# Optimization experiments

Measured on AMD Instinct MI355X. Metric: run time of the kernel, lower is better.

The kernel has to match this reference:

```python
import jax, jax.numpy as jnp
import numpy as np

N_HEADS = 16
D_MODEL = 1024
D_K = D_MODEL // N_HEADS


def setup_inputs() -> dict:
    key = jax.random.key(0)
    ks = jax.random.split(key, 9)
    B, L = 4, 2048
    s = 1.0 / np.sqrt(D_MODEL)
    x = jax.random.normal(ks[0], (B, L, D_MODEL), dtype=jnp.float32)
    mask = jnp.tril(jnp.ones((L, L), dtype=jnp.int32))  # causal [L, L]
    Wq = jax.random.normal(ks[1], (D_MODEL, D_MODEL), dtype=jnp.float32) * s
    Wk = jax.random.normal(ks[2], (D_MODEL, D_MODEL), dtype=jnp.float32) * s
    Wv = jax.random.normal(ks[3], (D_MODEL, D_MODEL), dtype=jnp.float32) * s
    Wo = jax.random.normal(ks[4], (D_MODEL, D_MODEL), dtype=jnp.float32) * s
    bq = jnp.zeros((D_MODEL,), jnp.float32)
    bk = jnp.zeros((D_MODEL,), jnp.float32)
    bv = jnp.zeros((D_MODEL,), jnp.float32)
    bo = jnp.zeros((D_MODEL,), jnp.float32)
    return {"x": x, "mask": mask, "Wq": Wq, "bq": bq, "Wk": Wk, "bk": bk,
            "Wv": Wv, "bv": bv, "Wo": Wo, "bo": bo}


def reference(x, mask, Wq, bq, Wk, bk, Wv, bv, Wo, bo):
    B, L, _ = x.shape
    # projections -> [B, H, L, d_k]
    def split_heads(t):
        return t.reshape(B, L, N_HEADS, D_K).transpose(0, 2, 1, 3)
    Q = split_heads(x @ Wq + bq)
    K = split_heads(x @ Wk + bk)
    V = split_heads(x @ Wv + bv)
    orig_dtype = Q.dtype
    # fp32 upcast for scores (faithful to source)
    scores = jnp.einsum('bhqd,bhkd->bhqk', Q.astype(jnp.float32),
                        K.astype(jnp.float32)) / np.sqrt(D_K)
    # orig dtype is float32 -> masked fill with -inf
    scores = jnp.where(mask == 0, -jnp.inf, scores).astype(orig_dtype)
    attn = jax.nn.softmax(scores, axis=-1)  # dropout p=0 -> identity (eval)
    out = jnp.einsum('bhqk,bhkd->bhqd', attn, V)
    out = out.transpose(0, 2, 1, 3).reshape(B, L, D_MODEL)
    return out @ Wo + bo
```

## Files before the change

### kernel.cpp

```cpp
#include <hip/hip_runtime.h>

#define DMODEL 1024
#define NTOK   8192
#define SEQ    2048
#define NH     16
#define DK     64

typedef short short8  __attribute__((ext_vector_type(8)));
typedef short short4v __attribute__((ext_vector_type(4)));
typedef float floatx4 __attribute__((ext_vector_type(4)));

__device__ __forceinline__ unsigned short f2bf(float f) {
  unsigned int u = __float_as_uint(f);
  u += 0x7fffu + ((u >> 16) & 1u);
  return (unsigned short)(u >> 16);
}

__device__ __forceinline__ void async16(short* lds, const short* g) {
  __builtin_amdgcn_global_load_lds(
      (const __attribute__((address_space(1))) void*)g,
      (__attribute__((address_space(3))) void*)lds, 16, 0, 0);
}

__global__ void cast_x_kernel(const float4* __restrict__ x, ushort4* __restrict__ o, int n4) {
  int i = blockIdx.x * 256 + threadIdx.x;
  if (i < n4) {
    float4 v = x[i];
    ushort4 u;
    u.x = f2bf(v.x); u.y = f2bf(v.y); u.z = f2bf(v.z); u.w = f2bf(v.w);
    o[i] = u;
  }
}

__global__ void transpose_cast4(const float* __restrict__ W0, const float* __restrict__ W1,
                                const float* __restrict__ W2, const float* __restrict__ W3,
                                short* __restrict__ T0, short* __restrict__ T1,
                                short* __restrict__ T2, short* __restrict__ T3) {
  __shared__ float tile[32][33];
  const int z = blockIdx.z;
  const float* W = (z == 0) ? W0 : (z == 1) ? W1 : (z == 2) ? W2 : W3;
  short*      Wt = (z == 0) ? T0 : (z == 1) ? T1 : (z == 2) ? T2 : T3;
  int bx = blockIdx.x, by = blockIdx.y;
  int tx = threadIdx.x, ty = threadIdx.y;
#pragma unroll
  for (int j = 0; j < 4; ++j)
    tile[ty + j * 8][tx] = W[(size_t)(by * 32 + ty + j * 8) * DMODEL + bx * 32 + tx];
  __syncthreads();
#pragma unroll
  for (int j = 0; j < 4; ++j)
    Wt[(size_t)(bx * 32 + ty + j * 8) * DMODEL + by * 32 + tx] =
        (short)f2bf(tile[tx][ty + j * 8]);
}

__global__ __launch_bounds__(256) void transpose_v(const short* __restrict__ Vb,
                                                   short* __restrict__ Vt) {
  __shared__ short t[64][72];
  const int bh = blockIdx.y, l0 = blockIdx.x * 64;
  const int tid = threadIdx.x;
  const int r = tid >> 2, c0 = (tid & 3) * 16;
  const short* src = Vb + (size_t)bh * SEQ * DK + (size_t)(l0 + r) * DK + c0;
  *(short8*)&t[r][c0]     = *(const short8*)src;
  *(short8*)&t[r][c0 + 8] = *(const short8*)(src + 8);
  __syncthreads();
  short tmp[16];
#pragma unroll
  for (int j = 0; j < 16; ++j) tmp[j] = t[c0 + j][r];
  short* dst = Vt + (size_t)bh * DK * SEQ + (size_t)r * SEQ + l0 + c0;
  *(short8*)dst       = *(const short8*)tmp;
  *(short8*)(dst + 8) = *(const short8*)(tmp + 8);
}

__device__ __forceinline__ void gemm_core(const short* __restrict__ A,
                                          const short* __restrict__ Bt,
                                          int m0, int n0, short* lds,
                                          floatx4 acc[4][4]) {
  const int tid  = threadIdx.x;
  const int lane = tid & 63, w = tid >> 6;
  const int wm = w >> 1, wn = w & 1;
  const int ln = lane & 15, quad = lane >> 4;
  short* As = lds;
  short* Bs = lds + 4096;
  const int   srow = tid >> 2;
  const int   scol = (tid & 3) * 8;
  const short* ga = A  + (size_t)(m0 + srow) * DMODEL + scol;
  const short* gb = Bt + (size_t)(n0 + srow) * DMODEL + scol;
  short* la = As + w * 512;
  short* lb = Bs + w * 512;
  for (int kb = 0; kb < DMODEL; kb += 32) {
    __syncthreads();
    async16(la,        ga + kb);
    async16(la + 2048, ga + (size_t)64 * DMODEL + kb);
    async16(lb,        gb + kb);
    async16(lb + 2048, gb + (size_t)64 * DMODEL + kb);
    __syncthreads();
    short8 af[4], bf[4];
#pragma unroll
    for (int t = 0; t < 4; ++t) {
      af[t] = *(const short8*)(As + (wm * 64 + t * 16 + ln) * 32 + quad * 8);
      bf[t] = *(const short8*)(Bs + (wn * 64 + t * 16 + ln) * 32 + quad * 8);
    }
#pragma unroll
    for (int mt = 0; mt < 4; ++mt)
#pragma unroll
      for (int nt = 0; nt < 4; ++nt)
        acc[mt][nt] = __builtin_amdgcn_mfma_f32_16x16x32_bf16(af[mt], bf[nt], acc[mt][nt], 0, 0, 0);
  }
}

__global__ __launch_bounds__(256) void gemm_qkv(
    const short* __restrict__ xb,
    const short* __restrict__ Wqt, const short* __restrict__ Wkt, const short* __restrict__ Wvt,
    const float* __restrict__ bq,  const float* __restrict__ bk,  const float* __restrict__ bv,
    short* __restrict__ Qb, short* __restrict__ Kb, short* __restrict__ Vb) {
  __shared__ __align__(16) short lds[8192];
  const int z = blockIdx.z;
  const short* Wt   = (z == 0) ? Wqt : (z == 1) ? Wkt : Wvt;
  const float* bias = (z == 0) ? bq  : (z == 1) ? bk  : bv;
  short* out        = (z == 0) ? Qb  : (z == 1) ? Kb  : Vb;
  const float scale = (z == 0) ? 0.18033688011112042f : 1.0f;
  const int m0 = blockIdx.y * 128, n0 = blockIdx.x * 128;
  floatx4 acc[4][4];
#pragma unroll
  for (int i = 0; i < 4; ++i)
#pragma unroll
    for (int j = 0; j < 4; ++j) acc[i][j] = (floatx4){0.f, 0.f, 0.f, 0.f};
  gemm_core(xb, Wt, m0, n0, lds, acc);
  const int tid = threadIdx.x, lane = tid & 63, w = tid >> 6;
  const int wm = w >> 1, wn = w & 1, ln = lane & 15, quad = lane >> 4;
#pragma unroll
  for (int mt = 0; mt < 4; ++mt)
#pragma unroll
    for (int nt = 0; nt < 4; ++nt) {
      int n = n0 + wn * 64 + nt * 16 + ln;
      float bb = bias[n];
      int h = n >> 6, d = n & 63;
#pragma unroll
      for (int r = 0; r < 4; ++r) {
        int m = m0 + wm * 64 + mt * 16 + quad * 4 + r;
        float v = (acc[mt][nt][r] + bb) * scale;
        int b = m >> 11, l = m & 2047;
        out[(size_t)(b * NH + h) * (SEQ * DK) + (size_t)l * DK + d] = (short)f2bf(v);
      }
    }
}

__global__ __launch_bounds__(256) void gemm_out(
    const short* __restrict__ Ob, const short* __restrict__ Wot,
    const float* __restrict__ bo, float* __restrict__ outp) {
  __shared__ __align__(16) short lds[8192];
  const int m0 = blockIdx.y * 128, n0 = blockIdx.x * 128;
  floatx4 acc[4][4];
#pragma unroll
  for (int i = 0; i < 4; ++i)
#pragma unroll
    for (int j = 0; j < 4; ++j) acc[i][j] = (floatx4){0.f, 0.f, 0.f, 0.f};
  gemm_core(Ob, Wot, m0, n0, lds, acc);
  const int tid = threadIdx.x, lane = tid & 63, w = tid >> 6;
  const int wm = w >> 1, wn = w & 1, ln = lane & 15, quad = lane >> 4;
#pragma unroll
  for (int mt = 0; mt < 4; ++mt)
#pragma unroll
    for (int nt = 0; nt < 4; ++nt) {
      int n = n0 + wn * 64 + nt * 16 + ln;
      float bb = bo[n];
#pragma unroll
      for (int r = 0; r < 4; ++r) {
        int m = m0 + wm * 64 + mt * 16 + quad * 4 + r;
        outp[(size_t)m * DMODEL + n] = acc[mt][nt][r] + bb;
      }
    }
}

#define FMAX 12.0f

__device__ __forceinline__ void attn_tile(
    const short* __restrict__ Ksb, const short* __restrict__ Vsb,
    short* __restrict__ Psg, const short8 qf[2][2],
    floatx4 acc[4][2], float lst[2],
    int qbase, int kt, int ln, int quad, int w) {
  floatx4 s[4][2];
#pragma unroll
  for (int i = 0; i < 4; ++i)
#pragma unroll
    for (int j = 0; j < 2; ++j) s[i][j] = (floatx4){0.f, 0.f, 0.f, 0.f};
#pragma unroll
  for (int kk = 0; kk < 2; ++kk) {
    short8 kf[4];
#pragma unroll
    for (int t = 0; t < 4; ++t)
      kf[t] = *(const short8*)(Ksb + (t * 16 + ln) * 64 + ((kk * 4 + quad) ^ (ln & 7)) * 8);
#pragma unroll
    for (int t = 0; t < 4; ++t)
#pragma unroll
      for (int qt = 0; qt < 2; ++qt)
        s[t][qt] = __builtin_amdgcn_mfma_f32_16x16x32_bf16(kf[t], qf[qt][kk], s[t][qt], 0, 0, 0);
  }
  if (kt * 64 + 63 > qbase) {
#pragma unroll
    for (int t = 0; t < 4; ++t)
#pragma unroll
      for (int qt = 0; qt < 2; ++qt)
#pragma unroll
        for (int r = 0; r < 4; ++r) {
          int kg = kt * 64 + t * 16 + quad * 4 + r;
          int qg = qbase + w * 32 + qt * 16 + ln;
          if (kg > qg) s[t][qt][r] = -1.0e30f;
        }
  }
#pragma unroll
  for (int qt = 0; qt < 2; ++qt) {
    float rs = 0.f;
#pragma unroll
    for (int t = 0; t < 4; ++t) {
      short4v pk;
#pragma unroll
      for (int r = 0; r < 4; ++r) {
        float p = __builtin_amdgcn_exp2f(s[t][qt][r] - FMAX);
        rs += p;
        pk[r] = (short)f2bf(p);
      }
      *(short4v*)(Psg + (w * 32 + qt * 16 + ln) * 72 + t * 16 + quad * 4) = pk;
    }
    lst[qt] += rs;
  }
  __threadfence_block();
#pragma unroll
  for (int kk = 0; kk < 2; ++kk) {
    short8 vf[4], pf[2];
#pragma unroll
    for (int dt = 0; dt < 4; ++dt)
      vf[dt] = *(const short8*)(Vsb + (dt * 16 + ln) * 64 + ((kk * 4 + quad) ^ (ln & 7)) * 8);
#pragma unroll
    for (int qt = 0; qt < 2; ++qt)
      pf[qt] = *(const short8*)(Psg + (w * 32 + qt * 16 + ln) * 72 + kk * 32 + quad * 8);
#pragma unroll
    for (int dt = 0; dt < 4; ++dt)
#pragma unroll
      for (int qt = 0; qt < 2; ++qt)
        acc[dt][qt] = __builtin_amdgcn_mfma_f32_16x16x32_bf16(vf[dt], pf[qt], acc[dt][qt], 0, 0, 0);
  }
}

__global__ __launch_bounds__(256, 2) void attn_kernel(
    const short* __restrict__ Qb, const short* __restrict__ Kb,
    const short* __restrict__ Vt, short* __restrict__ Ob) {
  __shared__ __align__(16) short Ks[2][64 * 64];
  __shared__ __align__(16) short Vs[2][64 * 64];
  __shared__ __align__(16) short Ps[2][128 * 72];
  const int tid = threadIdx.x, lane = tid & 63, w = tid >> 6;
  const int ln = lane & 15, quad = lane >> 4;
  const int pr  = blockIdx.x;
  const int qt0L = pr, qt0H = 15 - pr;
  const int bh  = blockIdx.y;
  const short* Qh = Qb + (size_t)bh * (SEQ * DK);
  const short* Kh = Kb + (size_t)bh * (SEQ * DK);
  const short* Vh = Vt + (size_t)bh * (DK * SEQ);

  short8 qfL[2][2], qfH[2][2];
#pragma unroll
  for (int qt = 0; qt < 2; ++qt)
#pragma unroll
    for (int kk = 0; kk < 2; ++kk) {
      qfL[qt][kk] = *(const short8*)(Qh +
          (size_t)(qt0L * 128 + w * 32 + qt * 16 + ln) * DK + kk * 32 + quad * 8);
      qfH[qt][kk] = *(const short8*)(Qh +
          (size_t)(qt0H * 128 + w * 32 + qt * 16 + ln) * DK + kk * 32 + quad * 8);
    }

  floatx4 accL[4][2], accH[4][2];
#pragma unroll
  for (int i = 0; i < 4; ++i)
#pragma unroll
    for (int j = 0; j < 2; ++j) {
      accL[i][j] = (floatx4){0.f, 0.f, 0.f, 0.f};
      accH[i][j] = (floatx4){0.f, 0.f, 0.f, 0.f};
    }
  float lstL[2] = {0.f, 0.f}, lstH[2] = {0.f, 0.f};

  const int lr = lane >> 3, fch = (lane & 7) ^ lr;
  const int nkt = 2 * qt0H + 2;
  const int nlt = 2 * qt0L + 2;

#pragma unroll
  for (int i = 0; i < 2; ++i) {
    int row = w * 16 + i * 8;
    async16(&Ks[0][row * 64], Kh + (size_t)(row + lr) * DK + fch * 8);
    async16(&Vs[0][row * 64], Vh + (size_t)(row + lr) * SEQ + fch * 8);
  }
  for (int kt = 0; kt < nkt; ++kt) {
    const int cur = kt & 1;
    __syncthreads();
    if (kt + 1 < nkt) {
      const short* Kt = Kh + (size_t)(kt + 1) * 64 * DK;
#pragma unroll
      for (int i = 0; i < 2; ++i) {
        int row = w * 16 + i * 8;
        async16(&Ks[cur ^ 1][row * 64], Kt + (size_t)(row + lr) * DK + fch * 8);
        async16(&Vs[cur ^ 1][row * 64],
                Vh + (size_t)(row + lr) * SEQ + (kt + 1) * 64 + fch * 8);
      }
    }
    if (kt < nlt)
      attn_tile(Ks[cur], Vs[cur], Ps[0], qfL, accL, lstL, qt0L * 128, kt, ln, quad, w);
    attn_tile(Ks[cur], Vs[cur], Ps[1], qfH, accH, lstH, qt0H * 128, kt, ln, quad, w);
  }

#pragma unroll
  for (int qt = 0; qt < 2; ++qt) {
    float lL = lstL[qt];
    lL += __shfl_xor(lL, 16); lL += __shfl_xor(lL, 32);
    float lH = lstH[qt];
    lH += __shfl_xor(lH, 16); lH += __shfl_xor(lH, 32);
    float invL = 1.0f / lL, invH = 1.0f / lH;
#pragma unroll
    for (int dt = 0; dt < 4; ++dt) {
      short4v oL, oH;
#pragma unroll
      for (int r = 0; r < 4; ++r) {
        oL[r] = (short)f2bf(accL[dt][qt][r] * invL);
        oH[r] = (short)f2bf(accH[dt][qt][r] * invH);
      }
      *(short4v*)(Ps[0] + (w * 32 + qt * 16 + ln) * 72 + dt * 16 + quad * 4) = oL;
      *(short4v*)(Ps[1] + (w * 32 + qt * 16 + ln) * 72 + dt * 16 + quad * 4) = oH;
    }
  }
  __syncthreads();
  const int b = bh >> 4, h = bh & 15;
  const int row = tid >> 1, c0 = (tid & 1) * 32;
  {
    short* dst = Ob + (size_t)(b * SEQ + qt0L * 128 + row) * DMODEL + h * DK + c0;
    const short* srcp = Ps[0] + row * 72 + c0;
#pragma unroll
    for (int u = 0; u < 4; ++u) *(short8*)(dst + u * 8) = *(const short8*)(srcp + u * 8);
  }
  {
    short* dst = Ob + (size_t)(b * SEQ + qt0H * 128 + row) * DMODEL + h * DK + c0;
    const short* srcp = Ps[1] + row * 72 + c0;
#pragma unroll
    for (int u = 0; u < 4; ++u) *(short8*)(dst + u * 8) = *(const short8*)(srcp + u * 8);
  }
}

extern "C" void kernel_launch(void* const* d_in, const int* in_sizes, int n_in,
                              void* d_out, int out_size, void* d_ws, size_t ws_size,
                              hipStream_t stream) {
  (void)in_sizes; (void)n_in; (void)out_size; (void)ws_size;
  const float* x  = (const float*)d_in[0];
  const float* Wq = (const float*)d_in[2];
  const float* bq = (const float*)d_in[3];
  const float* Wk = (const float*)d_in[4];
  const float* bk = (const float*)d_in[5];
  const float* Wv = (const float*)d_in[6];
  const float* bv = (const float*)d_in[7];
  const float* Wo = (const float*)d_in[8];
  const float* bo = (const float*)d_in[9];

  char* ws = (char*)d_ws;
  short* xb  = (short*)(ws);
  short* Vtg = (short*)(ws);
  short* Wqt = (short*)(ws + ((size_t)16 << 20));
  short* Wkt = (short*)(ws + ((size_t)18 << 20));
  short* Wvt = (short*)(ws + ((size_t)20 << 20));
  short* Wot = (short*)(ws + ((size_t)22 << 20));
  short* Qb  = (short*)(ws + ((size_t)24 << 20));
  short* Kb  = (short*)(ws + ((size_t)40 << 20));
  short* Vb  = (short*)(ws + ((size_t)56 << 20));
  short* Ob  = (short*)(ws + ((size_t)72 << 20));

  cast_x_kernel<<<NTOK * DMODEL / 4 / 256, 256, 0, stream>>>(
      (const float4*)x, (ushort4*)xb, NTOK * DMODEL / 4);
  transpose_cast4<<<dim3(32, 32, 4), dim3(32, 8), 0, stream>>>(
      Wq, Wk, Wv, Wo, Wqt, Wkt, Wvt, Wot);

  gemm_qkv<<<dim3(DMODEL / 128, NTOK / 128, 3), 256, 0, stream>>>(
      xb, Wqt, Wkt, Wvt, bq, bk, bv, Qb, Kb, Vb);

  transpose_v<<<dim3(SEQ / 64, 4 * NH), 256, 0, stream>>>(Vb, Vtg);

  attn_kernel<<<dim3(8, 4 * NH), 256, 0, stream>>>(Qb, Kb, Vtg, Ob);

  gemm_out<<<dim3(DMODEL / 128, NTOK / 128), 256, 0, stream>>>(Ob, Wot, bo, (float*)d_out);
}
```

Baseline: 292.8 us.

## Fuse Q/K/V projections into one GEMM and write V transposed directly

Replaces the three-way z-grid QKV GEMM with a single kernel that loads each x tile once and computes Q, K and V accumulators together, sharing the A fragment across three B tiles. The V epilogue writes straight into the transposed [B,H,DK,L] layout with packed 4-element stores, which removes the separate transpose_v kernel and its extra round trip through memory. The fused kernel holds 192 accumulator floats per thread and uses more LDS, so register pressure and occupancy are a risk. The grid also shrinks from 1536 to 512 blocks.

```diff
diff --git a/kernel.cpp b/kernel.cpp
--- a/kernel.cpp
+++ b/kernel.cpp
@@ -52,38 +52,118 @@
         (short)f2bf(tile[tx][ty + j * 8]);
 }
 
-__global__ __launch_bounds__(256) void transpose_v(const short* __restrict__ Vb,
-                                                   short* __restrict__ Vt) {
-  __shared__ short t[64][72];
-  const int bh = blockIdx.y, l0 = blockIdx.x * 64;
-  const int tid = threadIdx.x;
-  const int r = tid >> 2, c0 = (tid & 3) * 16;
-  const short* src = Vb + (size_t)bh * SEQ * DK + (size_t)(l0 + r) * DK + c0;
-  *(short8*)&t[r][c0]     = *(const short8*)src;
-  *(short8*)&t[r][c0 + 8] = *(const short8*)(src + 8);
-  __syncthreads();
-  short tmp[16];
-#pragma unroll
-  for (int j = 0; j < 16; ++j) tmp[j] = t[c0 + j][r];
-  short* dst = Vt + (size_t)bh * DK * SEQ + (size_t)r * SEQ + l0 + c0;
-  *(short8*)dst       = *(const short8*)tmp;
-  *(short8*)(dst + 8) = *(const short8*)(tmp + 8);
-}
-
-__device__ __forceinline__ void gemm_core(const short* __restrict__ A,
-                                          const short* __restrict__ Bt,
-                                          int m0, int n0, short* lds,
-                                          floatx4 acc[4][4]) {
-  const int tid  = threadIdx.x;
-  const int lane = tid & 63, w = tid >> 6;
-  const int wm = w >> 1, wn = w & 1;
-  const int ln = lane & 15, quad = lane >> 4;
+__global__ __launch_bounds__(256, 2) void gemm_qkv_fused(
+    const short* __restrict__ xb,
+    const short* __restrict__ Wqt, const short* __restrict__ Wkt, const short* __restrict__ Wvt,
+    const float* __restrict__ bq,  const float* __restrict__ bk,  const float* __restrict__ bv,
+    short* __restrict__ Qb, short* __restrict__ Kb, short* __restrict__ Vt) {
+  __shared__ __align__(16) short As[4096];
+  __shared__ __align__(16) short Bs[3][4096];
+  const int tid = threadIdx.x, lane = tid & 63, w = tid >> 6;
+  const int wm = w >> 1, wn = w & 1, ln = lane & 15, quad = lane >> 4;
+  const int m0 = blockIdx.y * 128, n0 = blockIdx.x * 128;
+
+  floatx4 acc[3][4][4];
+#pragma unroll
+  for (int z = 0; z < 3; ++z)
+#pragma unroll
+    for (int i = 0; i < 4; ++i)
+#pragma unroll
+      for (int j = 0; j < 4; ++j) acc[z][i][j] = (floatx4){0.f, 0.f, 0.f, 0.f};
+
+  const int srow = tid >> 2, scol = (tid & 3) * 8;
+  const short* ga  = xb  + (size_t)(m0 + srow) * DMODEL + scol;
+  const short* gb0 = Wqt + (size_t)(n0 + srow) * DMODEL + scol;
+  const short* gb1 = Wkt + (size_t)(n0 + srow) * DMODEL + scol;
+  const short* gb2 = Wvt + (size_t)(n0 + srow) * DMODEL + scol;
+  short* la  = As    + w * 512;
+  short* lb0 = Bs[0] + w * 512;
+  short* lb1 = Bs[1] + w * 512;
+  short* lb2 = Bs[2] + w * 512;
+
+  for (int kb = 0; kb < DMODEL; kb += 32) {
+    __syncthreads();
+    async16(la,         ga  + kb);
+    async16(la  + 2048, ga  + (size_t)64 * DMODEL + kb);
+    async16(lb0,        gb0 + kb);
+    async16(lb0 + 2048, gb0 + (size_t)64 * DMODEL + kb);
+    async16(lb1,        gb1 + kb);
+    async16(lb1 + 2048, gb1 + (size_t)64 * DMODEL + kb);
+    async16(lb2,        gb2 + kb);
+    async16(lb2 + 2048, gb2 + (size_t)64 * DMODEL + kb);
+    __syncthreads();
+    short8 af[4];
+#pragma unroll
+    for (int t = 0; t < 4; ++t)
+      af[t] = *(const short8*)(As + (wm * 64 + t * 16 + ln) * 32 + quad * 8);
+#pragma unroll
+    for (int z = 0; z < 3; ++z) {
+      short8 bf[4];
+#pragma unroll
+      for (int t = 0; t < 4; ++t)
+        bf[t] = *(const short8*)(Bs[z] + (wn * 64 + t * 16 + ln) * 32 + quad * 8);
+#pragma unroll
+      for (int mt = 0; mt < 4; ++mt)
+#pragma unroll
+        for (int nt = 0; nt < 4; ++nt)
+          acc[z][mt][nt] = __builtin_amdgcn_mfma_f32_16x16x32_bf16(af[mt], bf[nt], acc[z][mt][nt], 0, 0, 0);
+    }
+  }
+
+#pragma unroll
+  for (int z = 0; z < 2; ++z) {
+    const float* bias = z ? bk : bq;
+    short* out        = z ? Kb : Qb;
+    const float scale = z ? 1.0f : 0.18033688011112042f;
+#pragma unroll
+    for (int mt = 0; mt < 4; ++mt)
+#pragma unroll
+      for (int nt = 0; nt < 4; ++nt) {
+        int n = n0 + wn * 64 + nt * 16 + ln;
+        float bb = bias[n];
+        int h = n >> 6, d = n & 63;
+#pragma unroll
+        for (int r = 0; r < 4; ++r) {
+          int m = m0 + wm * 64 + mt * 16 + quad * 4 + r;
+          int b = m >> 11, l = m & 2047;
+          out[(size_t)(b * NH + h) * (SEQ * DK) + (size_t)l * DK + d] =
+              (short)f2bf((acc[z][mt][nt][r] + bb) * scale);
+        }
+      }
+  }
+#pragma unroll
+  for (int mt = 0; mt < 4; ++mt)
+#pragma unroll
+    for (int nt = 0; nt < 4; ++nt) {
+      int n = n0 + wn * 64 + nt * 16 + ln;
+      float bb = bv[n];
+      int h = n >> 6, d = n & 63;
+      int mb = m0 + wm * 64 + mt * 16 + quad * 4;
+      int b = mb >> 11, l = mb & 2047;
+      short4v pk;
+#pragma unroll
+      for (int r = 0; r < 4; ++r) pk[r] = (short)f2bf(acc[2][mt][nt][r] + bb);
+      *(short4v*)(Vt + ((size_t)(b * NH + h) * DK + d) * SEQ + l) = pk;
+    }
+}
+
+__global__ __launch_bounds__(256) void gemm_out(
+    const short* __restrict__ Ob, const short* __restrict__ Wot,
+    const float* __restrict__ bo, float* __restrict__ outp) {
+  __shared__ __align__(16) short lds[8192];
+  const int tid = threadIdx.x, lane = tid & 63, w = tid >> 6;
+  const int wm = w >> 1, wn = w & 1, ln = lane & 15, quad = lane >> 4;
+  const int m0 = blockIdx.y * 128, n0 = blockIdx.x * 128;
+  floatx4 acc[4][4];
+#pragma unroll
+  for (int i = 0; i < 4; ++i)
+#pragma unroll
+    for (int j = 0; j < 4; ++j) acc[i][j] = (floatx4){0.f, 0.f, 0.f, 0.f};
   short* As = lds;
   short* Bs = lds + 4096;
-  const int   srow = tid >> 2;
-  const int   scol = (tid & 3) * 8;
-  const short* ga = A  + (size_t)(m0 + srow) * DMODEL + scol;
-  const short* gb = Bt + (size_t)(n0 + srow) * DMODEL + scol;
+  const int srow = tid >> 2, scol = (tid & 3) * 8;
+  const short* ga = Ob  + (size_t)(m0 + srow) * DMODEL + scol;
+  const short* gb = Wot + (size_t)(n0 + srow) * DMODEL + scol;
   short* la = As + w * 512;
   short* lb = Bs + w * 512;
   for (int kb = 0; kb < DMODEL; kb += 32) {
@@ -105,58 +185,6 @@
       for (int nt = 0; nt < 4; ++nt)
         acc[mt][nt] = __builtin_amdgcn_mfma_f32_16x16x32_bf16(af[mt], bf[nt], acc[mt][nt], 0, 0, 0);
   }
-}
-
-__global__ __launch_bounds__(256) void gemm_qkv(
-    const short* __restrict__ xb,
-    const short* __restrict__ Wqt, const short* __restrict__ Wkt, const short* __restrict__ Wvt,
-    const float* __restrict__ bq,  const float* __restrict__ bk,  const float* __restrict__ bv,
-    short* __restrict__ Qb, short* __restrict__ Kb, short* __restrict__ Vb) {
-  __shared__ __align__(16) short lds[8192];
-  const int z = blockIdx.z;
-  const short* Wt   = (z == 0) ? Wqt : (z == 1) ? Wkt : Wvt;
-  const float* bias = (z == 0) ? bq  : (z == 1) ? bk  : bv;
-  short* out        = (z == 0) ? Qb  : (z == 1) ? Kb  : Vb;
-  const float scale = (z == 0) ? 0.18033688011112042f : 1.0f;
-  const int m0 = blockIdx.y * 128, n0 = blockIdx.x * 128;
-  floatx4 acc[4][4];
-#pragma unroll
-  for (int i = 0; i < 4; ++i)
-#pragma unroll
-    for (int j = 0; j < 4; ++j) acc[i][j] = (floatx4){0.f, 0.f, 0.f, 0.f};
-  gemm_core(xb, Wt, m0, n0, lds, acc);
-  const int tid = threadIdx.x, lane = tid & 63, w = tid >> 6;
-  const int wm = w >> 1, wn = w & 1, ln = lane & 15, quad = lane >> 4;
-#pragma unroll
-  for (int mt = 0; mt < 4; ++mt)
-#pragma unroll
-    for (int nt = 0; nt < 4; ++nt) {
-      int n = n0 + wn * 64 + nt * 16 + ln;
-      float bb = bias[n];
-      int h = n >> 6, d = n & 63;
-#pragma unroll
-      for (int r = 0; r < 4; ++r) {
-        int m = m0 + wm * 64 + mt * 16 + quad * 4 + r;
-        float v = (acc[mt][nt][r] + bb) * scale;
-        int b = m >> 11, l = m & 2047;
-        out[(size_t)(b * NH + h) * (SEQ * DK) + (size_t)l * DK + d] = (short)f2bf(v);
-      }
-    }
-}
-
-__global__ __launch_bounds__(256) void gemm_out(
-    const short* __restrict__ Ob, const short* __restrict__ Wot,
-    const float* __restrict__ bo, float* __restrict__ outp) {
-  __shared__ __align__(16) short lds[8192];
-  const int m0 = blockIdx.y * 128, n0 = blockIdx.x * 128;
-  floatx4 acc[4][4];
-#pragma unroll
-  for (int i = 0; i < 4; ++i)
-#pragma unroll
-    for (int j = 0; j < 4; ++j) acc[i][j] = (floatx4){0.f, 0.f, 0.f, 0.f};
-  gemm_core(Ob, Wot, m0, n0, lds, acc);
-  const int tid = threadIdx.x, lane = tid & 63, w = tid >> 6;
-  const int wm = w >> 1, wn = w & 1, ln = lane & 15, quad = lane >> 4;
 #pragma unroll
   for (int mt = 0; mt < 4; ++mt)
 #pragma unroll
@@ -357,14 +385,13 @@
 
   char* ws = (char*)d_ws;
   short* xb  = (short*)(ws);
-  short* Vtg = (short*)(ws);
   short* Wqt = (short*)(ws + ((size_t)16 << 20));
   short* Wkt = (short*)(ws + ((size_t)18 << 20));
   short* Wvt = (short*)(ws + ((size_t)20 << 20));
   short* Wot = (short*)(ws + ((size_t)22 << 20));
   short* Qb  = (short*)(ws + ((size_t)24 << 20));
   short* Kb  = (short*)(ws + ((size_t)40 << 20));
-  short* Vb  = (short*)(ws + ((size_t)56 << 20));
+  short* Vtg = (short*)(ws + ((size_t)56 << 20));
   short* Ob  = (short*)(ws + ((size_t)72 << 20));
 
   cast_x_kernel<<<NTOK * DMODEL / 4 / 256, 256, 0, stream>>>(
@@ -372,10 +399,8 @@
   transpose_cast4<<<dim3(32, 32, 4), dim3(32, 8), 0, stream>>>(
       Wq, Wk, Wv, Wo, Wqt, Wkt, Wvt, Wot);
 
-  gemm_qkv<<<dim3(DMODEL / 128, NTOK / 128, 3), 256, 0, stream>>>(
-      xb, Wqt, Wkt, Wvt, bq, bk, bv, Qb, Kb, Vb);
-
-  transpose_v<<<dim3(SEQ / 64, 4 * NH), 256, 0, stream>>>(Vb, Vtg);
+  gemm_qkv_fused<<<dim3(DMODEL / 128, NTOK / 128), 256, 0, stream>>>(
+      xb, Wqt, Wkt, Wvt, bq, bk, bv, Qb, Kb, Vtg);
 
   attn_kernel<<<dim3(8, 4 * NH), 256, 0, stream>>>(Qb, Kb, Vtg, Ob);
 
```

New measurement: 271.0 us. 7.5% less time.
